# Performance work log

Hardware: AMD Instinct MI355X
Metric: run time of the kernel (lower is better)

## Reference

```python
import jax, jax.numpy as jnp
import numpy as np

B, S, D, H = 64, 256, 2048, 16
HD = D // H  # 128
MAXS = 256


def setup_inputs() -> dict:
    key = jax.random.key(0)
    ks = jax.random.split(key, 16)
    sc = 0.02
    inp = {
        "q": jax.random.normal(ks[0], (B, S, D), jnp.float32),
        "k": jax.random.normal(ks[1], (B, S, D), jnp.float32),
        "v": jax.random.normal(ks[2], (B, S, D), jnp.float32),
        "attention_mask": jax.random.randint(ks[3], (B, S), 0, 2, jnp.int32),
        # projection weights, torch Linear convention: y = x @ W.T + b
        "Wq": jax.random.normal(ks[4], (D, D), jnp.float32) * sc,
        "bq": jnp.zeros((D,), jnp.float32),
        "Wk": jax.random.normal(ks[5], (D, D), jnp.float32) * sc,
        "bk": jnp.zeros((D,), jnp.float32),
        "Wv": jax.random.normal(ks[6], (D, D), jnp.float32) * sc,
        "bv": jnp.zeros((D,), jnp.float32),
        "Wo": jax.random.normal(ks[7], (D, D), jnp.float32) * sc,
        "bo": jnp.zeros((D,), jnp.float32),
        # additive per-head bias table (max_sequence_length=256)
        "bias_table": jax.random.normal(ks[8], (H, MAXS, MAXS), jnp.float32) * 0.1,
    }
    return inp


def reference(q, k, v, attention_mask, Wq, bq, Wk, bk, Wv, bv, Wo, bo, bias_table):
    def proj(x, W, b):  # (B,S,D) -> (B,H,S,HD)
        y = x @ W.T + b
        return y.reshape(B, S, H, HD).transpose(0, 2, 1, 3)

    qh = proj(q, Wq, bq)
    kh = proj(k, Wk, bk)
    vh = proj(v, Wv, bv)

    # (B,H,Sq,Sk) scores
    scores = jnp.einsum("bhqd,bhkd->bhqk", qh, kh) / jnp.sqrt(jnp.float32(HD))
    scores = scores + bias_table[None, :, :S, :S]
    # mask: (B,Sk) -> (B,1,1,Sk); masked_fill where mask==0
    neg_inf = jnp.finfo(scores.dtype).min
    scores = jnp.where(attention_mask[:, None, None, :] == 0, neg_inf, scores)
    probs = jax.nn.softmax(scores, axis=-1)  # dropout p=0.0 -> identity
    out = jnp.einsum("bhqk,bhkd->bhqd", probs, vh)
    out = out.transpose(0, 2, 1, 3).reshape(B, S, D)
    return out @ Wo.T + bo
```

## Files before the change

kernel.cpp:

```cpp
#include <hip/hip_runtime.h>
#include <hip/hip_bf16.h>

typedef __attribute__((ext_vector_type(4))) float f32x4;
typedef __attribute__((ext_vector_type(8))) short s16x8;
typedef __attribute__((ext_vector_type(4))) unsigned short u16x4;
typedef __attribute__((ext_vector_type(8))) unsigned short u16x8;
typedef __attribute__((ext_vector_type(4))) int i32x4;

#define NB 64
#define NS 256
#define ND 2048
#define NH 16
#define NHD 128

__device__ __forceinline__ unsigned short f2bf(float f){
  unsigned int u = __float_as_uint(f);
  u += 0x7fffu + ((u >> 16) & 1u);
  return (unsigned short)(u >> 16);
}

__device__ __forceinline__ void gload16(const void* g, void* l){
  __builtin_amdgcn_global_load_lds(
    (const __attribute__((address_space(1))) unsigned int*)g,
    (__attribute__((address_space(3))) unsigned int*)l, 16, 0, 0);
}

#define SBAR()  __builtin_amdgcn_sched_barrier(0)
#define BARRIER() do{ SBAR(); __builtin_amdgcn_s_barrier(); SBAR(); }while(0)
#define WAIT_LGKM0() do{ asm volatile("s_waitcnt lgkmcnt(0)" ::: "memory"); SBAR(); }while(0)
#define WAIT_VM0()   do{ asm volatile("s_waitcnt vmcnt(0)"   ::: "memory"); SBAR(); }while(0)
#define WAIT_VM4()   do{ asm volatile("s_waitcnt vmcnt(4)"   ::: "memory"); SBAR(); }while(0)
#define WAIT_VM8()   do{ asm volatile("s_waitcnt vmcnt(8)"   ::: "memory"); SBAR(); }while(0)

__global__ __launch_bounds__(256) void wconv(const float* __restrict__ s,
                                             unsigned short* __restrict__ d, int n8){
  int i = blockIdx.x*256 + threadIdx.x;
  if (i >= n8) return;
  f32x4 a = *(const f32x4*)(s + (size_t)i*8);
  f32x4 b = *(const f32x4*)(s + (size_t)i*8 + 4);
  u16x8 u;
  #pragma unroll
  for (int r=0;r<4;r++){ u[r]=f2bf(a[r]); u[4+r]=f2bf(b[r]); }
  *(u16x8*)(d + (size_t)i*8) = u;
}

__global__ __launch_bounds__(256) void wconv4(
  const float* __restrict__ s0, const float* __restrict__ s1,
  const float* __restrict__ s2, const float* __restrict__ s3,
  unsigned short* __restrict__ d0, unsigned short* __restrict__ d1,
  unsigned short* __restrict__ d2, unsigned short* __restrict__ d3)
{
  int j = blockIdx.x >> 11;
  const float* s = (j==0)?s0:(j==1)?s1:(j==2)?s2:s3;
  unsigned short* d = (j==0)?d0:(j==1)?d1:(j==2)?d2:d3;
  int i = (blockIdx.x & 2047)*256 + threadIdx.x;
  f32x4 a = *(const f32x4*)(s + (size_t)i*8);
  f32x4 b = *(const f32x4*)(s + (size_t)i*8 + 4);
  u16x8 u;
  #pragma unroll
  for (int r=0;r<4;r++){ u[r]=f2bf(a[r]); u[4+r]=f2bf(b[r]); }
  *(u16x8*)(d + (size_t)i*8) = u;
}

#define GEMM_COMMON_DECLS \
  extern __shared__ __attribute__((aligned(16))) char ldsb[]; \
  const int tid  = threadIdx.x; \
  const int lane = tid & 63, wid = tid >> 6; \
  const int g = lane >> 4, l15 = lane & 15; \
  const int wm = wid >> 2, wn = wid & 3; \
  const int nwg = gridDim.x, bid = blockIdx.x; \
  const int swz = (bid & 7) * (nwg >> 3) + (bid >> 3); \
  const int mt = swz >> 3, nt = swz & 7; \
  const int m0 = mt*256, n0 = nt*256; \
  const int srow_l = tid >> 3, slot = tid & 7;

#define RD_A(buf, qa) do{ \
    _Pragma("unroll") for (int i_=0;i_<4;i_++){ \
      int hr = (qa)*64 + i_*16 + l15; \
      const char* p_ = ldsb + (buf)*65536 + wm*16384 + hr*128; \
      _Pragma("unroll") for (int ks_=0;ks_<2;ks_++) \
        av[i_][ks_] = *(const s16x8*)(p_ + (((ks_*4+g) ^ (hr&7))*16)); } }while(0)

#define RD_B(buf, dst, qb) do{ \
    _Pragma("unroll") for (int j_=0;j_<2;j_++){ \
      int hc = (wn&1)*64 + (qb)*32 + j_*16 + l15; \
      const char* p_ = ldsb + (buf)*65536 + 32768 + (wn>>1)*16384 + hc*128; \
      _Pragma("unroll") for (int ks_=0;ks_<2;ks_++) \
        dst[j_][ks_] = *(const s16x8*)(p_ + (((ks_*4+g) ^ (hc&7))*16)); } }while(0)

#define MFMA_PH(qa, qb, bv) do{ \
    __builtin_amdgcn_s_setprio(1); \
    _Pragma("unroll") for (int i_=0;i_<4;i_++) \
      _Pragma("unroll") for (int j_=0;j_<2;j_++) \
        _Pragma("unroll") for (int ks_=0;ks_<2;ks_++) \
          acc[(qa)*4+i_][(qb)*2+j_] = __builtin_amdgcn_mfma_f32_16x16x32_bf16( \
              av[i_][ks_], bv[j_][ks_], acc[(qa)*4+i_][(qb)*2+j_], 0,0,0); \
    __builtin_amdgcn_s_setprio(0); }while(0)

#define GEMM_EPILOGUE(OUTMODE_) \
  _Pragma("unroll") \
  for (int jx=0;jx<4;jx++){ \
    int n = n0 + wn*64 + ((jx>>1)<<5) + ((jx&1)<<4) + l15; \
    float bj = bias[n]; \
    _Pragma("unroll") \
    for (int i=0;i<8;i++){ \
      int mb = m0 + wm*128 + ((i>>2)<<6) + ((i&3)<<4) + g*4; \
      if ((OUTMODE_) == 2){ \
        float* O = (float*)Out; \
        _Pragma("unroll") for (int r=0;r<4;r++) O[(size_t)(mb+r)*ND + n] = acc[i][jx][r] + bj; \
      } else if ((OUTMODE_) == 0){ \
        unsigned short* O = (unsigned short*)Out; \
        int bb = mb >> 8, h = n >> 7, d = n & 127, s0 = mb & 255; \
        _Pragma("unroll") for (int r=0;r<4;r++) \
          O[(((size_t)bb*NH + h)*NS + s0 + r)*NHD + d] = f2bf(acc[i][jx][r] + bj); \
      } else { \
        unsigned short* O = (unsigned short*)Out; \
        int bb = mb >> 8, h = n >> 7, d = n & 127, s0 = mb & 255; \
        u16x4 u; \
        _Pragma("unroll") for (int r=0;r<4;r++) u[r] = f2bf(acc[i][jx][r] + bj); \
        *(u16x4*)(O + (((size_t)bb*NH + h)*NHD + d)*NS + s0) = u; \
      } \
    } \
  }

template<int OUTMODE>
__global__ __launch_bounds__(512, 2) void gemm256(
    const unsigned short* __restrict__ A, const unsigned short* __restrict__ Bw,
    const float* __restrict__ bias, void* __restrict__ Out)
{
  GEMM_COMMON_DECLS
  const int scol = ((slot ^ (srow_l & 7)) * 8);
  const unsigned short* gsrc[4];
  gsrc[0] = A  + (size_t)(m0 +       srow_l)*ND + scol;
  gsrc[1] = A  + (size_t)(m0 + 128 + srow_l)*ND + scol;
  gsrc[2] = Bw + (size_t)(n0 +       srow_l)*ND + scol;
  gsrc[3] = Bw + (size_t)(n0 + 128 + srow_l)*ND + scol;

#define STAGE(buf, p, kt) do{ \
    const unsigned short* s_ = gsrc[p] + (kt); \
    char* d_ = ldsb + (buf)*65536 + ((p)>>1)*32768 + ((p)&1)*16384 + tid*16; \
    gload16(s_, d_); gload16(s_ + (size_t)64*ND, d_ + 8192); }while(0)

#define HALF(d, ktA, ktB, wmode) do{ \
    RD_A(d,0); RD_B(d,bva,0); \
    if ((ktA)>=0) STAGE((d)^1, 0, ktA); \
    WAIT_LGKM0(); \
    MFMA_PH(0,0,bva); \
    BARRIER(); \
    RD_B(d,bvb,1); \
    if ((ktA)>=0) STAGE((d)^1, 1, ktA); \
    WAIT_LGKM0(); \
    MFMA_PH(0,1,bvb); \
    BARRIER(); \
    RD_A(d,1); \
    if ((ktB)>=0) STAGE(d, 2, ktB); \
    WAIT_LGKM0(); \
    MFMA_PH(1,0,bva); \
    BARRIER(); \
    if ((ktB)>=0) STAGE(d, 3, ktB); \
    MFMA_PH(1,1,bvb); \
    if ((wmode)==0){ WAIT_VM4(); } \
    else if ((wmode)==1){ WAIT_VM0(); } \
    BARRIER(); \
  }while(0)

  f32x4 acc[8][4];
  s16x8 av[4][2], bva[2][2], bvb[2][2];

  STAGE(0,0,0); STAGE(0,1,0); STAGE(0,2,0); STAGE(0,3,0);
  STAGE(1,2,64); STAGE(1,3,64);
  #pragma unroll
  for (int i=0;i<8;i++)
    #pragma unroll
    for (int j=0;j<4;j++) acc[i][j] = f32x4{0.f,0.f,0.f,0.f};
  WAIT_VM4();
  BARRIER();

  for (int t = 0; t < 15; ++t) {
    HALF(0, (2*t+1)*64, (2*t+2)*64, 0);
    HALF(1, (2*t+2)*64, (2*t+3)*64, 0);
  }
  HALF(0, 31*64, -1, 1);
  HALF(1, -1, -1, -1);

  GEMM_EPILOGUE(OUTMODE)
#undef STAGE
#undef HALF
}

__global__ __launch_bounds__(512, 1) void attn_fused2(
  const unsigned short* __restrict__ Qh, const unsigned short* __restrict__ Kh,
  const unsigned short* __restrict__ VT, const int* __restrict__ mask,
  const float* __restrict__ bias_table, unsigned short* __restrict__ AO)
{
  __shared__ unsigned short Klds[256*128];
  __shared__ unsigned short Vlds[128*256];
  char* Kb_ = (char*)Klds; char* Vb_ = (char*)Vlds;
  const int bh = blockIdx.x, b = bh >> 4, h = bh & 15;
  const int tid = threadIdx.x, lane = tid & 63, w = tid >> 6;
  const int g = lane >> 4, l15 = lane & 15;

  {
    const unsigned short* Ksrc = Kh + (size_t)bh*NS*NHD;
    int r0 = tid >> 4, sl = tid & 15;
    #pragma unroll
    for (int c=0;c<8;c++){
      int row = c*32 + r0;
      gload16(Ksrc + (size_t)row*NHD + ((sl ^ (row&7))*8), Kb_ + c*8192 + tid*16);
    }
  }
  {
    const unsigned short* Vsrc = VT + (size_t)bh*NHD*NS;
    int r0 = tid >> 5, sl = tid & 31;
    #pragma unroll
    for (int c=0;c<8;c++){
      int row = c*16 + r0;
      gload16(Vsrc + (size_t)row*NS + ((sl ^ (row&7))*8), Vb_ + c*8192 + tid*16);
    }
  }
  WAIT_VM8();
  BARRIER();

  const float scale = 0.08838834764831845f;
  const int* mrow = mask + b*NS;
  const int s0l = l15 + ((g&1)<<5), s1l = s0l + 16;
  const int sel = g >> 1;

  auto pass = [&](int p, bool wait_v){
    const int q = w*32 + p*16 + l15;
    const unsigned short* Qrow = Qh + ((size_t)bh*NS + q)*NHD;
    s16x8 bq[4];
    #pragma unroll
    for (int kk=0;kk<4;kk++) bq[kk] = *(const s16x8*)(Qrow + kk*32 + g*8);

    f32x4 c[16];
    __builtin_amdgcn_s_setprio(1);
    #pragma unroll
    for (int kb=0;kb<16;kb++){
      c[kb] = f32x4{0.f,0.f,0.f,0.f};
      int row = kb*16 + l15;
      #pragma unroll
      for (int kk=0;kk<4;kk++){
        s16x8 a = *(const s16x8*)(Kb_ + row*256 + (((kk*4+g) ^ (row&7))*16));
        c[kb] = __builtin_amdgcn_mfma_f32_16x16x32_bf16(a, bq[kk], c[kb], 0,0,0);
      }
    }
    __builtin_amdgcn_s_setprio(0);

    const float* brow = bias_table + ((size_t)h*NS + q)*NS;
    float mx = -3.0e38f;
    #pragma unroll
    for (int kb=0;kb<16;kb++){
      f32x4 b4 = *(const f32x4*)(brow + kb*16 + g*4);
      i32x4 m4 = *(const i32x4*)(mrow + kb*16 + g*4);
      #pragma unroll
      for (int r=0;r<4;r++){
        float val = (m4[r] != 0) ? (c[kb][r]*scale + b4[r]) : -3.0e38f;
        c[kb][r] = val;
        mx = fmaxf(mx, val);
      }
    }
    mx = fmaxf(mx, __shfl_xor(mx, 16));
    mx = fmaxf(mx, __shfl_xor(mx, 32));
    float sum = 0.f;
    #pragma unroll
    for (int kb=0;kb<16;kb++)
      #pragma unroll
      for (int r=0;r<4;r++){
        float pv = __expf(c[kb][r] - mx);
        c[kb][r] = pv; sum += pv;
      }
    sum += __shfl_xor(sum, 16);
    sum += __shfl_xor(sum, 32);
    float inv = 1.f / sum;

    unsigned int pk[16][2];
    #pragma unroll
    for (int kb=0;kb<16;kb++){
      pk[kb][0] = (unsigned int)f2bf(c[kb][0]*inv) | ((unsigned int)f2bf(c[kb][1]*inv) << 16);
      pk[kb][1] = (unsigned int)f2bf(c[kb][2]*inv) | ((unsigned int)f2bf(c[kb][3]*inv) << 16);
    }

    if (wait_v){ WAIT_VM0(); BARRIER(); }

    s16x8 pb[8];
    #pragma unroll
    for (int kk=0;kk<8;kk++){
      unsigned int e0 = (unsigned int)__shfl((int)pk[2*kk][0],   s0l);
      unsigned int e1 = (unsigned int)__shfl((int)pk[2*kk][1],   s0l);
      unsigned int e2 = (unsigned int)__shfl((int)pk[2*kk][0],   s1l);
      unsigned int e3 = (unsigned int)__shfl((int)pk[2*kk][1],   s1l);
      unsigned int o0 = (unsigned int)__shfl((int)pk[2*kk+1][0], s0l);
      unsigned int o1 = (unsigned int)__shfl((int)pk[2*kk+1][1], s0l);
      unsigned int o2 = (unsigned int)__shfl((int)pk[2*kk+1][0], s1l);
      unsigned int o3 = (unsigned int)__shfl((int)pk[2*kk+1][1], s1l);
      union { unsigned int wd[4]; s16x8 v; } u_;
      u_.wd[0] = sel ? o0 : e0; u_.wd[1] = sel ? o1 : e1;
      u_.wd[2] = sel ? o2 : e2; u_.wd[3] = sel ? o3 : e3;
      pb[kk] = u_.v;
    }

    f32x4 oacc[8];
    __builtin_amdgcn_s_setprio(1);
    #pragma unroll
    for (int dt=0;dt<8;dt++){
      oacc[dt] = f32x4{0.f,0.f,0.f,0.f};
      int row = dt*16 + l15;
      #pragma unroll
      for (int kk=0;kk<8;kk++){
        s16x8 a = *(const s16x8*)(Vb_ + row*512 + (((kk*4+g) ^ (row&7))*16));
        oacc[dt] = __builtin_amdgcn_mfma_f32_16x16x32_bf16(a, pb[kk], oacc[dt], 0,0,0);
      }
    }
    __builtin_amdgcn_s_setprio(0);

    #pragma unroll
    for (int dt=0;dt<8;dt++){
      u16x4 u;
      #pragma unroll
      for (int r=0;r<4;r++) u[r] = f2bf(oacc[dt][r]);
      *(u16x4*)(AO + ((size_t)b*NS + q)*ND + h*NHD + dt*16 + g*4) = u;
    }
  };

  pass(0, true);
  pass(1, false);
}

extern "C" void kernel_launch(void* const* d_in, const int* in_sizes, int n_in,
                              void* d_out, int out_size, void* d_ws, size_t ws_size,
                              hipStream_t stream)
{
  const float* q  = (const float*)d_in[0];
  const float* k  = (const float*)d_in[1];
  const float* v  = (const float*)d_in[2];
  const int* mask = (const int*)d_in[3];
  const float* Wq = (const float*)d_in[4];
  const float* bq = (const float*)d_in[5];
  const float* Wk = (const float*)d_in[6];
  const float* bk = (const float*)d_in[7];
  const float* Wv = (const float*)d_in[8];
  const float* bv = (const float*)d_in[9];
  const float* Wo = (const float*)d_in[10];
  const float* bo = (const float*)d_in[11];
  const float* bias_table = (const float*)d_in[12];

  char* ws = (char*)d_ws;
  unsigned short* Wqb = (unsigned short*)(ws + 0);
  unsigned short* Wkb = (unsigned short*)(ws + 8388608);
  unsigned short* Wvb = (unsigned short*)(ws + 16777216);
  unsigned short* Wob = (unsigned short*)(ws + 25165824);
  unsigned short* tmp = (unsigned short*)(ws + 33554432);
  unsigned short* Qh  = (unsigned short*)(ws + 100663296);
  unsigned short* Kh  = (unsigned short*)(ws + 167772160);
  unsigned short* VT  = (unsigned short*)(ws + 234881024);
  unsigned short* AO  = (unsigned short*)(ws + 301989888);

  hipFuncSetAttribute((const void*)gemm256<0>, hipFuncAttributeMaxDynamicSharedMemorySize, 131072);
  hipFuncSetAttribute((const void*)gemm256<1>, hipFuncAttributeMaxDynamicSharedMemorySize, 131072);
  hipFuncSetAttribute((const void*)gemm256<2>, hipFuncAttributeMaxDynamicSharedMemorySize, 131072);

  wconv4<<<8192,256,0,stream>>>(Wq,Wk,Wv,Wo, Wqb,Wkb,Wvb,Wob);

  const float* acts[3] = {q, k, v};
  const unsigned short* wgt[3] = {Wqb, Wkb, Wvb};
  const float* bia[3] = {bq, bk, bv};
  unsigned short* outs[3] = {Qh, Kh, VT};

  for (int x = 0; x < 3; ++x) {
    wconv<<<16384,256,0,stream>>>(acts[x], tmp, 4194304);
    if (x < 2)
      gemm256<0><<<512,512,131072,stream>>>(tmp, wgt[x], bia[x], outs[x]);
    else
      gemm256<1><<<512,512,131072,stream>>>(tmp, wgt[x], bia[x], outs[x]);
  }

  attn_fused2<<<1024,512,0,stream>>>(Qh,Kh,VT,mask,bias_table,AO);
  gemm256<2><<<512,512,131072,stream>>>(AO,Wob,bo,(float*)d_out);
}
```

Before: 731.1 us.

## Load V directly from global memory in attention to halve LDS and raise occupancy

The attention kernel no longer stages V^T in shared memory. Each wave loads its V fragments straight from global memory into registers before the PV MFMAs, and the launch bound is relaxed to allow multiple blocks per CU. This halves LDS use so more blocks can be co-resident, hiding latency across blocks. The trade is repeated V reads through the cache hierarchy instead of one shared LDS copy, plus added register pressure and global-load latency inside the MFMA loop.

```diff
diff --git a/kernel.cpp b/kernel.cpp
--- a/kernel.cpp
+++ b/kernel.cpp
@@ -30,7 +30,6 @@
 #define WAIT_LGKM0() do{ asm volatile("s_waitcnt lgkmcnt(0)" ::: "memory"); SBAR(); }while(0)
 #define WAIT_VM0()   do{ asm volatile("s_waitcnt vmcnt(0)"   ::: "memory"); SBAR(); }while(0)
 #define WAIT_VM4()   do{ asm volatile("s_waitcnt vmcnt(4)"   ::: "memory"); SBAR(); }while(0)
-#define WAIT_VM8()   do{ asm volatile("s_waitcnt vmcnt(8)"   ::: "memory"); SBAR(); }while(0)
 
 __global__ __launch_bounds__(256) void wconv(const float* __restrict__ s,
                                              unsigned short* __restrict__ d, int n8){
@@ -188,14 +187,13 @@
 #undef HALF
 }
 
-__global__ __launch_bounds__(512, 1) void attn_fused2(
+__global__ __launch_bounds__(512, 4) void attn_fused3(
   const unsigned short* __restrict__ Qh, const unsigned short* __restrict__ Kh,
   const unsigned short* __restrict__ VT, const int* __restrict__ mask,
   const float* __restrict__ bias_table, unsigned short* __restrict__ AO)
 {
   __shared__ unsigned short Klds[256*128];
-  __shared__ unsigned short Vlds[128*256];
-  char* Kb_ = (char*)Klds; char* Vb_ = (char*)Vlds;
+  char* Kb_ = (char*)Klds;
   const int bh = blockIdx.x, b = bh >> 4, h = bh & 15;
   const int tid = threadIdx.x, lane = tid & 63, w = tid >> 6;
   const int g = lane >> 4, l15 = lane & 15;
@@ -209,24 +207,16 @@
       gload16(Ksrc + (size_t)row*NHD + ((sl ^ (row&7))*8), Kb_ + c*8192 + tid*16);
     }
   }
-  {
-    const unsigned short* Vsrc = VT + (size_t)bh*NHD*NS;
-    int r0 = tid >> 5, sl = tid & 31;
-    #pragma unroll
-    for (int c=0;c<8;c++){
-      int row = c*16 + r0;
-      gload16(Vsrc + (size_t)row*NS + ((sl ^ (row&7))*8), Vb_ + c*8192 + tid*16);
-    }
-  }
-  WAIT_VM8();
+  WAIT_VM0();
   BARRIER();
 
   const float scale = 0.08838834764831845f;
   const int* mrow = mask + b*NS;
+  const unsigned short* Vsrc = VT + (size_t)bh*NHD*NS;
   const int s0l = l15 + ((g&1)<<5), s1l = s0l + 16;
   const int sel = g >> 1;
 
-  auto pass = [&](int p, bool wait_v){
+  auto pass = [&](int p){
     const int q = w*32 + p*16 + l15;
     const unsigned short* Qrow = Qh + ((size_t)bh*NS + q)*NHD;
     s16x8 bq[4];
@@ -280,8 +270,6 @@
       pk[kb][0] = (unsigned int)f2bf(c[kb][0]*inv) | ((unsigned int)f2bf(c[kb][1]*inv) << 16);
       pk[kb][1] = (unsigned int)f2bf(c[kb][2]*inv) | ((unsigned int)f2bf(c[kb][3]*inv) << 16);
     }
-
-    if (wait_v){ WAIT_VM0(); BARRIER(); }
 
     s16x8 pb[8];
     #pragma unroll
@@ -301,18 +289,19 @@
     }
 
     f32x4 oacc[8];
-    __builtin_amdgcn_s_setprio(1);
     #pragma unroll
     for (int dt=0;dt<8;dt++){
+      s16x8 va[8];
+      const unsigned short* vr = Vsrc + (size_t)(dt*16 + l15)*NS + g*8;
+      #pragma unroll
+      for (int kk=0;kk<8;kk++) va[kk] = *(const s16x8*)(vr + kk*32);
       oacc[dt] = f32x4{0.f,0.f,0.f,0.f};
-      int row = dt*16 + l15;
-      #pragma unroll
-      for (int kk=0;kk<8;kk++){
-        s16x8 a = *(const s16x8*)(Vb_ + row*512 + (((kk*4+g) ^ (row&7))*16));
-        oacc[dt] = __builtin_amdgcn_mfma_f32_16x16x32_bf16(a, pb[kk], oacc[dt], 0,0,0);
-      }
-    }
-    __builtin_amdgcn_s_setprio(0);
+      __builtin_amdgcn_s_setprio(1);
+      #pragma unroll
+      for (int kk=0;kk<8;kk++)
+        oacc[dt] = __builtin_amdgcn_mfma_f32_16x16x32_bf16(va[kk], pb[kk], oacc[dt], 0,0,0);
+      __builtin_amdgcn_s_setprio(0);
+    }
 
     #pragma unroll
     for (int dt=0;dt<8;dt++){
@@ -323,8 +312,8 @@
     }
   };
 
-  pass(0, true);
-  pass(1, false);
+  pass(0);
+  pass(1);
 }
 
 extern "C" void kernel_launch(void* const* d_in, const int* in_sizes, int n_in,
@@ -375,6 +364,6 @@
       gemm256<1><<<512,512,131072,stream>>>(tmp, wgt[x], bia[x], outs[x]);
   }
 
-  attn_fused2<<<1024,512,0,stream>>>(Qh,Kh,VT,mask,bias_table,AO);
+  attn_fused3<<<1024,512,0,stream>>>(Qh,Kh,VT,mask,bias_table,AO);
   gemm256<2><<<512,512,131072,stream>>>(AO,Wob,bo,(float*)d_out);
 }
```

Result: slower. 787.3 us (+7.7%).

## Split attention into 4 query tiles per head and reuse one LDS buffer for K then V

Applied to the files above, without the earlier changes.

The attention kernel now launches four 256-thread blocks per (batch, head), each handling 64 queries, instead of one 512-thread block doing two passes over 256 queries. A single 64KB LDS buffer holds K for the QK^T step and is then overwritten with V after a barrier, which halves shared memory per block so two blocks can share a CU. The aim is more occupancy and better latency hiding. In exchange, K and V are loaded from global memory four times per head instead of once, and the V load can no longer overlap the QK^T compute.

```diff
diff --git a/kernel.cpp b/kernel.cpp
--- a/kernel.cpp
+++ b/kernel.cpp
@@ -30,7 +30,6 @@
 #define WAIT_LGKM0() do{ asm volatile("s_waitcnt lgkmcnt(0)" ::: "memory"); SBAR(); }while(0)
 #define WAIT_VM0()   do{ asm volatile("s_waitcnt vmcnt(0)"   ::: "memory"); SBAR(); }while(0)
 #define WAIT_VM4()   do{ asm volatile("s_waitcnt vmcnt(4)"   ::: "memory"); SBAR(); }while(0)
-#define WAIT_VM8()   do{ asm volatile("s_waitcnt vmcnt(8)"   ::: "memory"); SBAR(); }while(0)
 
 __global__ __launch_bounds__(256) void wconv(const float* __restrict__ s,
                                              unsigned short* __restrict__ d, int n8){
@@ -188,143 +187,142 @@
 #undef HALF
 }
 
-__global__ __launch_bounds__(512, 1) void attn_fused2(
+__global__ __launch_bounds__(256, 2) void attn_fused4(
   const unsigned short* __restrict__ Qh, const unsigned short* __restrict__ Kh,
   const unsigned short* __restrict__ VT, const int* __restrict__ mask,
   const float* __restrict__ bias_table, unsigned short* __restrict__ AO)
 {
-  __shared__ unsigned short Klds[256*128];
-  __shared__ unsigned short Vlds[128*256];
-  char* Kb_ = (char*)Klds; char* Vb_ = (char*)Vlds;
-  const int bh = blockIdx.x, b = bh >> 4, h = bh & 15;
+  __shared__ unsigned short KV[256*128];
+  char* KVb = (char*)KV;
+  const int bh = blockIdx.x >> 2, qt = blockIdx.x & 3;
+  const int b = bh >> 4, h = bh & 15;
   const int tid = threadIdx.x, lane = tid & 63, w = tid >> 6;
   const int g = lane >> 4, l15 = lane & 15;
+  const int q = qt*64 + w*16 + l15;
 
   {
     const unsigned short* Ksrc = Kh + (size_t)bh*NS*NHD;
     int r0 = tid >> 4, sl = tid & 15;
     #pragma unroll
-    for (int c=0;c<8;c++){
-      int row = c*32 + r0;
-      gload16(Ksrc + (size_t)row*NHD + ((sl ^ (row&7))*8), Kb_ + c*8192 + tid*16);
-    }
-  }
+    for (int c=0;c<16;c++){
+      int row = c*16 + r0;
+      gload16(Ksrc + (size_t)row*NHD + ((sl ^ (row&7))*8), KVb + c*4096 + tid*16);
+    }
+  }
+  const unsigned short* Qrow = Qh + ((size_t)bh*NS + q)*NHD;
+  s16x8 bq[4];
+  #pragma unroll
+  for (int kk=0;kk<4;kk++) bq[kk] = *(const s16x8*)(Qrow + kk*32 + g*8);
+
+  WAIT_VM0();
+  BARRIER();
+
+  f32x4 c[16];
+  __builtin_amdgcn_s_setprio(1);
+  #pragma unroll
+  for (int kb=0;kb<16;kb++){
+    c[kb] = f32x4{0.f,0.f,0.f,0.f};
+    int row = kb*16 + l15;
+    #pragma unroll
+    for (int kk=0;kk<4;kk++){
+      s16x8 a = *(const s16x8*)(KVb + row*256 + (((kk*4+g) ^ (row&7))*16));
+      c[kb] = __builtin_amdgcn_mfma_f32_16x16x32_bf16(a, bq[kk], c[kb], 0,0,0);
+    }
+  }
+  __builtin_amdgcn_s_setprio(0);
+
+  WAIT_LGKM0();
+  BARRIER();
+
   {
     const unsigned short* Vsrc = VT + (size_t)bh*NHD*NS;
     int r0 = tid >> 5, sl = tid & 31;
     #pragma unroll
-    for (int c=0;c<8;c++){
-      int row = c*16 + r0;
-      gload16(Vsrc + (size_t)row*NS + ((sl ^ (row&7))*8), Vb_ + c*8192 + tid*16);
-    }
-  }
-  WAIT_VM8();
+    for (int c2=0;c2<16;c2++){
+      int row = c2*8 + r0;
+      gload16(Vsrc + (size_t)row*NS + ((sl ^ (row&7))*8), KVb + c2*4096 + tid*16);
+    }
+  }
+
+  const float scale = 0.08838834764831845f;
+  const float* brow = bias_table + ((size_t)h*NS + q)*NS;
+  const int*   mrow = mask + b*NS;
+  float mx = -3.0e38f;
+  #pragma unroll
+  for (int kb=0;kb<16;kb++){
+    f32x4 b4 = *(const f32x4*)(brow + kb*16 + g*4);
+    i32x4 m4 = *(const i32x4*)(mrow + kb*16 + g*4);
+    #pragma unroll
+    for (int r=0;r<4;r++){
+      float val = (m4[r] != 0) ? (c[kb][r]*scale + b4[r]) : -3.0e38f;
+      c[kb][r] = val;
+      mx = fmaxf(mx, val);
+    }
+  }
+  mx = fmaxf(mx, __shfl_xor(mx, 16));
+  mx = fmaxf(mx, __shfl_xor(mx, 32));
+  float sum = 0.f;
+  #pragma unroll
+  for (int kb=0;kb<16;kb++)
+    #pragma unroll
+    for (int r=0;r<4;r++){
+      float pv = __expf(c[kb][r] - mx);
+      c[kb][r] = pv; sum += pv;
+    }
+  sum += __shfl_xor(sum, 16);
+  sum += __shfl_xor(sum, 32);
+  float inv = 1.f / sum;
+
+  unsigned int pk[16][2];
+  #pragma unroll
+  for (int kb=0;kb<16;kb++){
+    pk[kb][0] = (unsigned int)f2bf(c[kb][0]*inv) | ((unsigned int)f2bf(c[kb][1]*inv) << 16);
+    pk[kb][1] = (unsigned int)f2bf(c[kb][2]*inv) | ((unsigned int)f2bf(c[kb][3]*inv) << 16);
+  }
+
+  WAIT_VM0();
   BARRIER();
 
-  const float scale = 0.08838834764831845f;
-  const int* mrow = mask + b*NS;
   const int s0l = l15 + ((g&1)<<5), s1l = s0l + 16;
   const int sel = g >> 1;
-
-  auto pass = [&](int p, bool wait_v){
-    const int q = w*32 + p*16 + l15;
-    const unsigned short* Qrow = Qh + ((size_t)bh*NS + q)*NHD;
-    s16x8 bq[4];
-    #pragma unroll
-    for (int kk=0;kk<4;kk++) bq[kk] = *(const s16x8*)(Qrow + kk*32 + g*8);
-
-    f32x4 c[16];
-    __builtin_amdgcn_s_setprio(1);
-    #pragma unroll
-    for (int kb=0;kb<16;kb++){
-      c[kb] = f32x4{0.f,0.f,0.f,0.f};
-      int row = kb*16 + l15;
-      #pragma unroll
-      for (int kk=0;kk<4;kk++){
-        s16x8 a = *(const s16x8*)(Kb_ + row*256 + (((kk*4+g) ^ (row&7))*16));
-        c[kb] = __builtin_amdgcn_mfma_f32_16x16x32_bf16(a, bq[kk], c[kb], 0,0,0);
-      }
-    }
-    __builtin_amdgcn_s_setprio(0);
-
-    const float* brow = bias_table + ((size_t)h*NS + q)*NS;
-    float mx = -3.0e38f;
-    #pragma unroll
-    for (int kb=0;kb<16;kb++){
-      f32x4 b4 = *(const f32x4*)(brow + kb*16 + g*4);
-      i32x4 m4 = *(const i32x4*)(mrow + kb*16 + g*4);
-      #pragma unroll
-      for (int r=0;r<4;r++){
-        float val = (m4[r] != 0) ? (c[kb][r]*scale + b4[r]) : -3.0e38f;
-        c[kb][r] = val;
-        mx = fmaxf(mx, val);
-      }
-    }
-    mx = fmaxf(mx, __shfl_xor(mx, 16));
-    mx = fmaxf(mx, __shfl_xor(mx, 32));
-    float sum = 0.f;
-    #pragma unroll
-    for (int kb=0;kb<16;kb++)
-      #pragma unroll
-      for (int r=0;r<4;r++){
-        float pv = __expf(c[kb][r] - mx);
-        c[kb][r] = pv; sum += pv;
-      }
-    sum += __shfl_xor(sum, 16);
-    sum += __shfl_xor(sum, 32);
-    float inv = 1.f / sum;
-
-    unsigned int pk[16][2];
-    #pragma unroll
-    for (int kb=0;kb<16;kb++){
-      pk[kb][0] = (unsigned int)f2bf(c[kb][0]*inv) | ((unsigned int)f2bf(c[kb][1]*inv) << 16);
-      pk[kb][1] = (unsigned int)f2bf(c[kb][2]*inv) | ((unsigned int)f2bf(c[kb][3]*inv) << 16);
-    }
-
-    if (wait_v){ WAIT_VM0(); BARRIER(); }
-
-    s16x8 pb[8];
+  s16x8 pb[8];
+  #pragma unroll
+  for (int kk=0;kk<8;kk++){
+    unsigned int e0 = (unsigned int)__shfl((int)pk[2*kk][0],   s0l);
+    unsigned int e1 = (unsigned int)__shfl((int)pk[2*kk][1],   s0l);
+    unsigned int e2 = (unsigned int)__shfl((int)pk[2*kk][0],   s1l);
+    unsigned int e3 = (unsigned int)__shfl((int)pk[2*kk][1],   s1l);
+    unsigned int o0 = (unsigned int)__shfl((int)pk[2*kk+1][0], s0l);
+    unsigned int o1 = (unsigned int)__shfl((int)pk[2*kk+1][1], s0l);
+    unsigned int o2 = (unsigned int)__shfl((int)pk[2*kk+1][0], s1l);
+    unsigned int o3 = (unsigned int)__shfl((int)pk[2*kk+1][1], s1l);
+    union { unsigned int wd[4]; s16x8 v; } u_;
+    u_.wd[0] = sel ? o0 : e0; u_.wd[1] = sel ? o1 : e1;
+    u_.wd[2] = sel ? o2 : e2; u_.wd[3] = sel ? o3 : e3;
+    pb[kk] = u_.v;
+  }
+
+  f32x4 oacc[8];
+  __builtin_amdgcn_s_setprio(1);
+  #pragma unroll
+  for (int dt=0;dt<8;dt++){
+    oacc[dt] = f32x4{0.f,0.f,0.f,0.f};
+    int row = dt*16 + l15;
     #pragma unroll
     for (int kk=0;kk<8;kk++){
-      unsigned int e0 = (unsigned int)__shfl((int)pk[2*kk][0],   s0l);
-      unsigned int e1 = (unsigned int)__shfl((int)pk[2*kk][1],   s0l);
-      unsigned int e2 = (unsigned int)__shfl((int)pk[2*kk][0],   s1l);
-      unsigned int e3 = (unsigned int)__shfl((int)pk[2*kk][1],   s1l);
-      unsigned int o0 = (unsigned int)__shfl((int)pk[2*kk+1][0], s0l);
-      unsigned int o1 = (unsigned int)__shfl((int)pk[2*kk+1][1], s0l);
-      unsigned int o2 = (unsigned int)__shfl((int)pk[2*kk+1][0], s1l);
-      unsigned int o3 = (unsigned int)__shfl((int)pk[2*kk+1][1], s1l);
-      union { unsigned int wd[4]; s16x8 v; } u_;
-      u_.wd[0] = sel ? o0 : e0; u_.wd[1] = sel ? o1 : e1;
-      u_.wd[2] = sel ? o2 : e2; u_.wd[3] = sel ? o3 : e3;
-      pb[kk] = u_.v;
-    }
-
-    f32x4 oacc[8];
-    __builtin_amdgcn_s_setprio(1);
-    #pragma unroll
-    for (int dt=0;dt<8;dt++){
-      oacc[dt] = f32x4{0.f,0.f,0.f,0.f};
-      int row = dt*16 + l15;
-      #pragma unroll
-      for (int kk=0;kk<8;kk++){
-        s16x8 a = *(const s16x8*)(Vb_ + row*512 + (((kk*4+g) ^ (row&7))*16));
-        oacc[dt] = __builtin_amdgcn_mfma_f32_16x16x32_bf16(a, pb[kk], oacc[dt], 0,0,0);
-      }
-    }
-    __builtin_amdgcn_s_setprio(0);
-
-    #pragma unroll
-    for (int dt=0;dt<8;dt++){
-      u16x4 u;
-      #pragma unroll
-      for (int r=0;r<4;r++) u[r] = f2bf(oacc[dt][r]);
-      *(u16x4*)(AO + ((size_t)b*NS + q)*ND + h*NHD + dt*16 + g*4) = u;
-    }
-  };
-
-  pass(0, true);
-  pass(1, false);
+      s16x8 a = *(const s16x8*)(KVb + row*512 + (((kk*4+g) ^ (row&7))*16));
+      oacc[dt] = __builtin_amdgcn_mfma_f32_16x16x32_bf16(a, pb[kk], oacc[dt], 0,0,0);
+    }
+  }
+  __builtin_amdgcn_s_setprio(0);
+
+  #pragma unroll
+  for (int dt=0;dt<8;dt++){
+    u16x4 u;
+    #pragma unroll
+    for (int r=0;r<4;r++) u[r] = f2bf(oacc[dt][r]);
+    *(u16x4*)(AO + ((size_t)b*NS + q)*ND + h*NHD + dt*16 + g*4) = u;
+  }
 }
 
 extern "C" void kernel_launch(void* const* d_in, const int* in_sizes, int n_in,
@@ -375,6 +373,6 @@
       gemm256<1><<<512,512,131072,stream>>>(tmp, wgt[x], bia[x], outs[x]);
   }
 
-  attn_fused2<<<1024,512,0,stream>>>(Qh,Kh,VT,mask,bias_table,AO);
+  attn_fused4<<<4096,256,0,stream>>>(Qh,Kh,VT,mask,bias_table,AO);
   gemm256<2><<<512,512,131072,stream>>>(AO,Wob,bo,(float*)d_out);
 }
```

New measurement: 739.4 us. No clear change (+1.1%).
